# Kernel tuning notes

Hardware: AMD Instinct MI355X
Metric: run time of the kernel (lower is better)

Reference implementation:

```python
import jax, jax.numpy as jnp
import numpy as np

WS = 8        # window_size
SS = 4        # shift_size
NH = 8        # num_heads
DIM = 256
HD = DIM // NH
SCALE = HD ** -0.5
EPS = 1e-5


def _rel_pos_index(ws):
    ch, cw = np.meshgrid(np.arange(ws), np.arange(ws), indexing='ij')
    coords = np.stack([ch.ravel(), cw.ravel()])            # [2, ws*ws]
    rel = coords[:, :, None] - coords[:, None, :]           # [2, N, N]
    rel = rel.transpose(1, 2, 0)
    rel[:, :, 0] += ws - 1
    rel[:, :, 1] += ws - 1
    rel[:, :, 0] *= 2 * ws - 1
    return jnp.asarray(rel.sum(-1))                         # [N, N] int

REL_IDX = _rel_pos_index(WS)


def _ln(x, g, b):
    m = jnp.mean(x, axis=-1, keepdims=True)
    v = jnp.mean(jnp.square(x - m), axis=-1, keepdims=True)
    return (x - m) * jax.lax.rsqrt(v + EPS) * g + b


def setup_inputs() -> dict:
    key = jax.random.key(0)
    ks = jax.random.split(key, 12)
    B, L, C = 8, 16384, DIM
    s = lambda k, shape, scale=0.02: jax.random.normal(k, shape, jnp.float32) * scale
    return {
        'x': jax.random.normal(ks[0], (B, L, C), jnp.float32),
        'norm1_g': jnp.ones((C,), jnp.float32),
        'norm1_b': jnp.zeros((C,), jnp.float32),
        'qkv_w': s(ks[1], (C, 3 * C)),
        'qkv_b': jnp.zeros((3 * C,), jnp.float32),
        'rel_bias': s(ks[2], ((2 * WS - 1) ** 2, NH)),
        'proj_w': s(ks[3], (C, C)),
        'proj_b': jnp.zeros((C,), jnp.float32),
        'norm2_g': jnp.ones((C,), jnp.float32),
        'norm2_b': jnp.zeros((C,), jnp.float32),
        'fc1_w': s(ks[4], (C, C)),
        'fc1_b': jnp.zeros((C,), jnp.float32),
        'fc2_w': s(ks[5], (C, C)),
        'fc2_b': jnp.zeros((C,), jnp.float32),
        'H': 128,
        'W': 128,
    }


def reference(x, norm1_g, norm1_b, qkv_w, qkv_b, rel_bias, proj_w, proj_b,
              norm2_g, norm2_b, fc1_w, fc1_b, fc2_w, fc2_b, H, W):
    B, L, C = x.shape
    shortcut = x
    h = _ln(x, norm1_g, norm1_b).reshape(B, H, W, C)
    pad_b = (WS - H % WS) % WS
    pad_r = (WS - W % WS) % WS
    h = jnp.pad(h, ((0, 0), (0, pad_b), (0, pad_r), (0, 0)))
    Hp, Wp = H + pad_b, W + pad_r
    if SS > 0:
        h = jnp.roll(h, (-SS, -SS), axis=(1, 2))
    # window partition -> [B*nW, WS*WS, C]
    h = h.reshape(B, Hp // WS, WS, Wp // WS, WS, C)
    h = h.transpose(0, 1, 3, 2, 4, 5).reshape(-1, WS * WS, C)
    Bn, N = h.shape[0], WS * WS
    # attention
    qkv = (h @ qkv_w + qkv_b).reshape(Bn, N, 3, NH, HD)
    q, k, v = qkv[:, :, 0], qkv[:, :, 1], qkv[:, :, 2]   # [Bn, N, NH, HD]
    attn = jnp.einsum('bnhd,bmhd->bhnm', q * SCALE, k)
    bias = rel_bias[REL_IDX.reshape(-1)].reshape(N, N, NH).transpose(2, 0, 1)
    attn = jax.nn.softmax(attn + bias[None], axis=-1)
    o = jnp.einsum('bhnm,bmhd->bnhd', attn, v).reshape(Bn, N, C)
    o = o @ proj_w + proj_b
    # window reverse
    o = o.reshape(B, Hp // WS, Wp // WS, WS, WS, C)
    o = o.transpose(0, 1, 3, 2, 4, 5).reshape(B, Hp, Wp, C)
    if SS > 0:
        o = jnp.roll(o, (SS, SS), axis=(1, 2))
    o = o[:, :H, :W, :].reshape(B, H * W, C)
    x = shortcut + o
    # MLP (hidden = dim, exact GELU as nn.GELU default)
    m = _ln(x, norm2_g, norm2_b)
    m = jax.nn.gelu(m @ fc1_w + fc1_b, approximate=False)
    m = m @ fc2_w + fc2_b
    return x + m
```

## Files before the change

### kernel.cpp

```cpp
#include <hip/hip_runtime.h>
#include <stdint.h>

typedef __bf16 bf16;
typedef __bf16 bf16x4v __attribute__((ext_vector_type(4)));
typedef __bf16 bf16x8 __attribute__((ext_vector_type(8)));
typedef float floatx4 __attribute__((ext_vector_type(4)));
typedef float float4v __attribute__((ext_vector_type(4)));

#define SCALE 0.17677669529663689f

__device__ __forceinline__ float ldin(const void* p, long i, int f32) {
  return f32 ? ((const float*)p)[i] : (float)(((const bf16*)p)[i]);
}

__device__ __forceinline__ void async16(const bf16* g, bf16* l) {
  __builtin_amdgcn_global_load_lds(
      (const __attribute__((address_space(1))) void*)g,
      (__attribute__((address_space(3))) void*)l, 16, 0, 0);
}

__global__ void detect_k(const unsigned short* __restrict__ x, int* flag) {
  __shared__ int cnt;
  if (threadIdx.x == 0) cnt = 0;
  __syncthreads();
  int local = 0;
  for (int i = threadIdx.x; i < 4096; i += 256) {
    unsigned short w = x[i];
    int e = (w >> 7) & 0xFF;
    if (w != 0 && (e >= 0x9F || e <= 0x5F)) local++;
  }
  atomicAdd(&cnt, local);
  __syncthreads();
  if (threadIdx.x == 0) *flag = (cnt >= 64) ? 1 : 0;
}

__global__ void conv_w_k(const void* __restrict__ W, bf16* __restrict__ Wt,
                         int K, int N, const int* __restrict__ flag) {
  int f32 = *flag;
  int idx = blockIdx.x * 256 + threadIdx.x;
  if (idx < K * N) {
    int k = idx / N, n = idx % N;
    Wt[n * K + k] = (bf16)ldin(W, idx, f32);
  }
}

__global__ void conv3_k(const void* __restrict__ W0, const void* __restrict__ W1,
                        const void* __restrict__ W2, bf16* __restrict__ T0,
                        bf16* __restrict__ T1, bf16* __restrict__ T2,
                        const int* __restrict__ flag) {
  int f32 = *flag;
  int which = blockIdx.x >> 8;
  int idx = (blockIdx.x & 255) * 256 + threadIdx.x;
  const void* W = which == 0 ? W0 : which == 1 ? W1 : W2;
  bf16* T = which == 0 ? T0 : which == 1 ? T1 : T2;
  int k = idx >> 8, n = idx & 255;
  T[n * 256 + k] = (bf16)ldin(W, idx, f32);
}

__global__ void bias_k(const void* __restrict__ rel, float* __restrict__ bias_s,
                       const int* __restrict__ flag) {
  int f = *flag;
  int idx = blockIdx.x * 256 + threadIdx.x;
  int r = idx & 3, ni = (idx >> 2) & 3, mi = (idx >> 4) & 3;
  int l16 = (idx >> 6) & 15, quad = (idx >> 10) & 3, head = idx >> 12;
  int i = mi * 16 + quad * 4 + r, j = ni * 16 + l16;
  int dy = (i >> 3) - (j >> 3) + 7, dx = (i & 7) - (j & 7) + 7;
  bias_s[idx] = ldin(rel, (dy * 15 + dx) * 8 + head, f);
}

__global__ __launch_bounds__(256) void ln_k(const void* __restrict__ x,
                                            const void* __restrict__ g,
                                            const void* __restrict__ b,
                                            bf16* __restrict__ y,
                                            const int* __restrict__ flag,
                                            int x_input) {
  int f = *flag;
  int f32x = x_input ? f : 0;
  int wave = threadIdx.x >> 6, lane = threadIdx.x & 63;
  long row = (long)blockIdx.x * 4 + wave;
  float v[4];
  if (f32x) {
    float4v u = ((const float4v*)x)[row * 64 + lane];
    for (int i = 0; i < 4; i++) v[i] = u[i];
  } else {
    bf16x4v u = ((const bf16x4v*)x)[row * 64 + lane];
    for (int i = 0; i < 4; i++) v[i] = (float)u[i];
  }
  float s = v[0] + v[1] + v[2] + v[3];
  for (int off = 32; off > 0; off >>= 1) s += __shfl_xor(s, off, 64);
  float mean = s * (1.f / 256.f);
  float q = 0.f;
  for (int i = 0; i < 4; i++) { float d = v[i] - mean; q += d * d; }
  for (int off = 32; off > 0; off >>= 1) q += __shfl_xor(q, off, 64);
  float rstd = rsqrtf(q * (1.f / 256.f) + 1e-5f);
  bf16x4v o;
  for (int i = 0; i < 4; i++) {
    float gv = ldin(g, lane * 4 + i, f);
    float bv = ldin(b, lane * 4 + i, f);
    o[i] = (bf16)((v[i] - mean) * rstd * gv + bv);
  }
  ((bf16x4v*)y)[row * 64 + lane] = o;
}

template <int EPI>
__global__ __launch_bounds__(256) void gemm_bt_k(
    const bf16* __restrict__ A, const bf16* __restrict__ Bt,
    const void* __restrict__ bias, const void* __restrict__ res,
    void* __restrict__ C, int M, int N, int K, const int* __restrict__ flag,
    int res_input, int out_input) {
  __shared__ __align__(16) char smem[32768];
  bf16* Sb = (bf16*)smem;
  float* CsF = (float*)smem;

  const int tid = threadIdx.x;
  const int ntiles = gridDim.x;
  int bid = blockIdx.y * ntiles + blockIdx.x;
  const int nwg = ntiles * gridDim.y;
  if (!(nwg & 7)) bid = (bid & 7) * (nwg >> 3) + (bid >> 3);
  const long m0 = (long)(bid / ntiles) * 128;
  const int n0 = (bid % ntiles) * 128;
  const int wave = tid >> 6, lane = tid & 63;
  const int wm = wave & 1, wn = wave >> 1;
  const int quad = lane >> 4, l16 = lane & 15;

  floatx4 acc[4][4];
  for (int i = 0; i < 4; i++)
    for (int j = 0; j < 4; j++) acc[i][j] = (floatx4){0.f, 0.f, 0.f, 0.f};

  const int ldr = tid >> 2;
  const int ldc = (((tid & 3) ^ ((tid >> 3) & 3)) << 3);

  const bf16* gA0 = A + (m0 + ldr) * K + ldc;
  const bf16* gA1 = A + (m0 + 64 + ldr) * K + ldc;
  const bf16* gB0 = Bt + (long)(n0 + ldr) * K + ldc;
  const bf16* gB1 = Bt + (long)(n0 + 64 + ldr) * K + ldc;

  const int rswz = (l16 >> 1) & 3;
  const int NT = K >> 5;

#define STAGE(b, tt)                                   \
  do {                                                 \
    bf16* _base = Sb + (b) * 8192 + wave * 512;        \
    int _kt = (tt) << 5;                               \
    async16(gA0 + _kt, _base);                         \
    async16(gA1 + _kt, _base + 2048);                  \
    async16(gB0 + _kt, _base + 4096);                  \
    async16(gB1 + _kt, _base + 6144);                  \
  } while (0)

  STAGE(0, 0);
  __syncthreads();

  int cur = 0;
  for (int t = 0; t < NT; ++t) {
    if (t + 1 < NT) STAGE(cur ^ 1, t + 1);
    const bf16* As_t = Sb + cur * 8192;
    const bf16* Bs_t = As_t + 4096;
    bf16x8 af[4], bfr[4];
    for (int mi = 0; mi < 4; mi++)
      af[mi] = *(const bf16x8*)&As_t[(wm * 64 + mi * 16 + l16) * 32 +
                                     ((quad ^ rswz) << 3)];
    for (int ni = 0; ni < 4; ni++)
      bfr[ni] = *(const bf16x8*)&Bs_t[(wn * 64 + ni * 16 + l16) * 32 +
                                      ((quad ^ rswz) << 3)];
    for (int mi = 0; mi < 4; mi++)
      for (int ni = 0; ni < 4; ni++)
        acc[mi][ni] = __builtin_amdgcn_mfma_f32_16x16x32_bf16(
            af[mi], bfr[ni], acc[mi][ni], 0, 0, 0);
    __syncthreads();
    cur ^= 1;
  }
#undef STAGE

  const int f = *flag;
  const int rf32 = res_input ? f : 0;
  const int of32 = out_input ? f : 0;
  for (int mi = 0; mi < 4; mi++) {
    __syncthreads();
    for (int ni = 0; ni < 4; ni++) {
      int col = n0 + wn * 64 + ni * 16 + l16;
      float bv = ldin(bias, col, f);
      for (int r = 0; r < 4; r++) {
        float v = acc[mi][ni][r] + bv;
        if (EPI == 1) v = v * 0.5f * (1.f + erff(v * 0.70710678118654752f));
        CsF[(wm * 16 + quad * 4 + r) * 132 + wn * 64 + ni * 16 + l16] = v;
      }
    }
    __syncthreads();
    const int s = tid >> 3;
    const int seg = tid & 7;
    const long grow = m0 + (s >> 4) * 64 + mi * 16 + (s & 15);
    const int gcol = n0 + seg * 16;
    const float4v* src = (const float4v*)&CsF[s * 132 + seg * 16];
    float4v v0 = src[0], v1 = src[1], v2 = src[2], v3 = src[3];
    if (EPI == 2) {
      if (rf32) {
        const float4v* rp = (const float4v*)((const float*)res + grow * N + gcol);
        v0 += rp[0]; v1 += rp[1]; v2 += rp[2]; v3 += rp[3];
      } else {
        const bf16x8* rp = (const bf16x8*)((const bf16*)res + grow * N + gcol);
        bf16x8 r0 = rp[0], r1 = rp[1];
        for (int j = 0; j < 4; j++) {
          v0[j] += (float)r0[j];     v1[j] += (float)r0[4 + j];
          v2[j] += (float)r1[j];     v3[j] += (float)r1[4 + j];
        }
      }
    }
    if (of32) {
      float4v* dst = (float4v*)((float*)C + grow * N + gcol);
      dst[0] = v0; dst[1] = v1; dst[2] = v2; dst[3] = v3;
    } else {
      bf16x8 o0, o1;
      for (int j = 0; j < 4; j++) {
        o0[j] = (bf16)v0[j]; o0[4 + j] = (bf16)v1[j];
        o1[j] = (bf16)v2[j]; o1[4 + j] = (bf16)v3[j];
      }
      bf16x8* dst = (bf16x8*)((bf16*)C + grow * N + gcol);
      dst[0] = o0; dst[1] = o1;
    }
  }
}

__global__ __launch_bounds__(256) void attn_k(const bf16* __restrict__ qkv,
                                              const float* __restrict__ bias_s,
                                              bf16* __restrict__ o) {
  __shared__ bf16 Pb[4][64 * 64];
  __shared__ bf16 Vb[4][32 * 64];
  const int tid = threadIdx.x;
  const int wave = tid >> 6, lane = tid & 63;
  const int quad = lane >> 4, l16 = lane & 15;
  const int gid = blockIdx.x * 4 + wave;
  const int head = gid & 7, win = gid >> 3;
  const int wx = win & 15, wy = (win >> 4) & 15, bb = win >> 8;

  bf16* P = Pb[wave];
  bf16* Vt = Vb[wave];

  bf16x8 qf[4], kf[4];
  for (int mi = 0; mi < 4; mi++) {
    int t = mi * 16 + l16;
    int rr = (wy * 8 + (t >> 3) + 4) & 127;
    int cc = (wx * 8 + (t & 7) + 4) & 127;
    long base = ((long)(bb * 16384 + rr * 128 + cc)) * 768 + head * 32 + quad * 8;
    qf[mi] = *(const bf16x8*)(qkv + base);
    kf[mi] = *(const bf16x8*)(qkv + base + 256);
    bf16x8 vv = *(const bf16x8*)(qkv + base + 512);
    int tcol = t ^ (quad << 4);
    for (int jj = 0; jj < 8; jj++) Vt[(quad * 8 + jj) * 64 + tcol] = vv[jj];
  }
  __syncthreads();

  floatx4 acc[4][4];
  for (int mi = 0; mi < 4; mi++)
    for (int ni = 0; ni < 4; ni++) {
      floatx4 z = (floatx4){0.f, 0.f, 0.f, 0.f};
      acc[mi][ni] = __builtin_amdgcn_mfma_f32_16x16x32_bf16(qf[mi], kf[ni], z, 0, 0, 0);
    }

  const float4v* bp =
      (const float4v*)(bias_s + (((head * 4 + quad) * 16 + l16) << 6));
  for (int mi = 0; mi < 4; mi++) {
    float mx[4] = {-1e30f, -1e30f, -1e30f, -1e30f};
    for (int ni = 0; ni < 4; ni++) {
      float4v bv = bp[mi * 4 + ni];
      for (int r = 0; r < 4; r++) {
        acc[mi][ni][r] = acc[mi][ni][r] * SCALE + bv[r];
        mx[r] = fmaxf(mx[r], acc[mi][ni][r]);
      }
    }
    for (int r = 0; r < 4; r++) {
      float m = mx[r];
      for (int off = 1; off < 16; off <<= 1) m = fmaxf(m, __shfl_xor(m, off, 64));
      mx[r] = m;
    }
    float sm[4] = {0.f, 0.f, 0.f, 0.f};
    for (int ni = 0; ni < 4; ni++)
      for (int r = 0; r < 4; r++) {
        float e = __expf(acc[mi][ni][r] - mx[r]);
        acc[mi][ni][r] = e;
        sm[r] += e;
      }
    for (int r = 0; r < 4; r++) {
      float s = sm[r];
      for (int off = 1; off < 16; off <<= 1) s += __shfl_xor(s, off, 64);
      sm[r] = 1.f / s;
    }
    for (int ni = 0; ni < 4; ni++)
      for (int r = 0; r < 4; r++) {
        int i = mi * 16 + quad * 4 + r;
        int j = ni * 16 + l16;
        P[i * 64 + (j ^ ((i & 7) << 3))] = (bf16)(acc[mi][ni][r] * sm[r]);
      }
  }
  __syncthreads();

  floatx4 oacc[4][2];
  for (int mi = 0; mi < 4; mi++)
    for (int nt = 0; nt < 2; nt++) oacc[mi][nt] = (floatx4){0.f, 0.f, 0.f, 0.f};
  for (int ks = 0; ks < 2; ks++) {
    bf16x8 vfr[2];
    for (int nt = 0; nt < 2; nt++) {
      int d = nt * 16 + l16;
      vfr[nt] =
          *(const bf16x8*)&Vt[d * 64 + ((ks * 32 + quad * 8) ^ ((d >> 3) << 4))];
    }
    for (int mi = 0; mi < 4; mi++) {
      int i = mi * 16 + l16;
      bf16x8 pf =
          *(const bf16x8*)&P[i * 64 + ((ks * 32 + quad * 8) ^ ((i & 7) << 3))];
      for (int nt = 0; nt < 2; nt++)
        oacc[mi][nt] = __builtin_amdgcn_mfma_f32_16x16x32_bf16(pf, vfr[nt],
                                                               oacc[mi][nt], 0, 0, 0);
    }
  }

  for (int mi = 0; mi < 4; mi++)
    for (int r = 0; r < 4; r++) {
      int t = mi * 16 + quad * 4 + r;
      int rot = (t >> 1) & 3;
      int c0 = l16, c1 = 16 + l16;
      Vt[t * 32 + ((((c0 >> 3) + rot) & 3) << 3) + (c0 & 7)] = (bf16)oacc[mi][0][r];
      Vt[t * 32 + ((((c1 >> 3) + rot) & 3) << 3) + (c1 & 7)] = (bf16)oacc[mi][1][r];
    }
  {
    int t = lane;
    int rot = (t >> 1) & 3;
    int rr = (wy * 8 + (t >> 3) + 4) & 127;
    int cc = (wx * 8 + (t & 7) + 4) & 127;
    long base = ((long)(bb * 16384 + rr * 128 + cc)) * 256 + head * 32;
    bf16x8* dst = (bf16x8*)(o + base);
    for (int k = 0; k < 4; k++)
      dst[k] = *(const bf16x8*)&Vt[t * 32 + (((k + rot) & 3) << 3)];
  }
}

extern "C" void kernel_launch(void* const* d_in, const int* in_sizes, int n_in,
                              void* d_out, int out_size, void* d_ws,
                              size_t ws_size, hipStream_t stream) {
  const void* x = d_in[0];
  const void* n1g = d_in[1];
  const void* n1b = d_in[2];
  const void* qkv_w = d_in[3];
  const void* qkv_b = d_in[4];
  const void* rel_bias = d_in[5];
  const void* proj_w = d_in[6];
  const void* proj_b = d_in[7];
  const void* n2g = d_in[8];
  const void* n2b = d_in[9];
  const void* fc1_w = d_in[10];
  const void* fc1_b = d_in[11];
  const void* fc2_w = d_in[12];
  const void* fc2_b = d_in[13];

  char* ws = (char*)d_ws;
  int* flag = (int*)ws;
  float* bias_s = (float*)(ws + 4096);
  bf16* qkvWt = (bf16*)(ws + 262144);
  bf16* projWt = qkvWt + 768 * 256;
  bf16* fc1Wt = projWt + 256 * 256;
  bf16* fc2Wt = fc1Wt + 256 * 256;
  bf16* reg1 = (bf16*)(ws + (1 << 20));
  bf16* reg2 = (bf16*)(ws + (1 << 20) + 67108864);

  const int M = 131072;

  detect_k<<<1, 256, 0, stream>>>((const unsigned short*)x, flag);

  bias_k<<<128, 256, 0, stream>>>(rel_bias, bias_s, flag);
  conv_w_k<<<768, 256, 0, stream>>>(qkv_w, qkvWt, 256, 768, flag);
  conv3_k<<<768, 256, 0, stream>>>(proj_w, fc1_w, fc2_w, projWt, fc1Wt, fc2Wt,
                                   flag);

  bf16* h = reg1;
  ln_k<<<M / 4, 256, 0, stream>>>(x, n1g, n1b, h, flag, 1);

  bf16* qkv = reg2;
  gemm_bt_k<0><<<dim3(6, M / 128), 256, 0, stream>>>(
      h, qkvWt, qkv_b, nullptr, qkv, M, 768, 256, flag, 0, 0);

  bf16* o = reg1;
  attn_k<<<2048 * 8 / 4, 256, 0, stream>>>(qkv, bias_s, o);

  bf16* x2 = reg2;
  gemm_bt_k<2><<<dim3(2, M / 128), 256, 0, stream>>>(
      o, projWt, proj_b, x, x2, M, 256, 256, flag, 1, 0);

  bf16* mbuf = reg1;
  ln_k<<<M / 4, 256, 0, stream>>>(x2, n2g, n2b, mbuf, flag, 0);

  bf16* m1 = reg2 + 33554432;
  gemm_bt_k<1><<<dim3(2, M / 128), 256, 0, stream>>>(
      mbuf, fc1Wt, fc1_b, nullptr, m1, M, 256, 256, flag, 0, 0);

  gemm_bt_k<2><<<dim3(2, M / 128), 256, 0, stream>>>(
      m1, fc2Wt, fc2_b, x2, d_out, M, 256, 256, flag, 0, 1);
}
```

Before: 740.9 us.

## Load GEMM B fragments directly from global into registers, halve LDS

The GEMM kernel no longer stages the B (weight) tile through LDS. Each wave now loads its B fragments straight from global memory into registers, double-buffered by unrolling the k-loop by two, while A stays in LDS. LDS shrinks from 32 KB to about 16.5 KB, which may allow more blocks per CU and removes the LDS reads for B. The cost is more register pressure and uncoalesced, redundant global loads of B across the waves that share it. The loop also assumes NT is handled correctly when odd, since the second half is skipped only through its guard.

Result: slower. 813.6 us (+9.8%).

```diff
diff --git a/kernel.cpp b/kernel.cpp
--- a/kernel.cpp
+++ b/kernel.cpp
@@ -108,7 +108,7 @@
     const void* __restrict__ bias, const void* __restrict__ res,
     void* __restrict__ C, int M, int N, int K, const int* __restrict__ flag,
     int res_input, int out_input) {
-  __shared__ __align__(16) char smem[32768];
+  __shared__ __align__(16) char smem[16896];
   bf16* Sb = (bf16*)smem;
   float* CsF = (float*)smem;
 
@@ -132,45 +132,56 @@
 
   const bf16* gA0 = A + (m0 + ldr) * K + ldc;
   const bf16* gA1 = A + (m0 + 64 + ldr) * K + ldc;
-  const bf16* gB0 = Bt + (long)(n0 + ldr) * K + ldc;
-  const bf16* gB1 = Bt + (long)(n0 + 64 + ldr) * K + ldc;
+  const bf16* gB = Bt + (long)(n0 + wn * 64 + l16) * K + quad * 8;
+  const long bstride = (long)16 * K;
 
   const int rswz = (l16 >> 1) & 3;
   const int NT = K >> 5;
 
-#define STAGE(b, tt)                                   \
+#define STAGE_A(b, tt)                                 \
   do {                                                 \
-    bf16* _base = Sb + (b) * 8192 + wave * 512;        \
+    bf16* _base = Sb + (b) * 4096 + wave * 512;        \
     int _kt = (tt) << 5;                               \
     async16(gA0 + _kt, _base);                         \
     async16(gA1 + _kt, _base + 2048);                  \
-    async16(gB0 + _kt, _base + 4096);                  \
-    async16(gB1 + _kt, _base + 6144);                  \
   } while (0)
 
-  STAGE(0, 0);
+#define BLOAD(dst, tt)                                                 \
+  do {                                                                 \
+    int _kt = (tt) << 5;                                               \
+    for (int _ni = 0; _ni < 4; _ni++)                                  \
+      dst[_ni] = *(const bf16x8*)(gB + _ni * bstride + _kt);           \
+  } while (0)
+
+#define COMPUTE(bufidx, bfrag)                                          \
+  do {                                                                  \
+    const bf16* As_t = Sb + (bufidx) * 4096;                            \
+    bf16x8 af[4];                                                       \
+    for (int mi = 0; mi < 4; mi++)                                      \
+      af[mi] = *(const bf16x8*)&As_t[(wm * 64 + mi * 16 + l16) * 32 +   \
+                                     ((quad ^ rswz) << 3)];             \
+    for (int mi = 0; mi < 4; mi++)                                      \
+      for (int ni = 0; ni < 4; ni++)                                    \
+        acc[mi][ni] = __builtin_amdgcn_mfma_f32_16x16x32_bf16(          \
+            af[mi], bfrag[ni], acc[mi][ni], 0, 0, 0);                   \
+  } while (0)
+
+  bf16x8 bf0[4], bf1[4];
+  STAGE_A(0, 0);
+  BLOAD(bf0, 0);
   __syncthreads();
 
-  int cur = 0;
-  for (int t = 0; t < NT; ++t) {
-    if (t + 1 < NT) STAGE(cur ^ 1, t + 1);
-    const bf16* As_t = Sb + cur * 8192;
-    const bf16* Bs_t = As_t + 4096;
-    bf16x8 af[4], bfr[4];
-    for (int mi = 0; mi < 4; mi++)
-      af[mi] = *(const bf16x8*)&As_t[(wm * 64 + mi * 16 + l16) * 32 +
-                                     ((quad ^ rswz) << 3)];
-    for (int ni = 0; ni < 4; ni++)
-      bfr[ni] = *(const bf16x8*)&Bs_t[(wn * 64 + ni * 16 + l16) * 32 +
-                                      ((quad ^ rswz) << 3)];
-    for (int mi = 0; mi < 4; mi++)
-      for (int ni = 0; ni < 4; ni++)
-        acc[mi][ni] = __builtin_amdgcn_mfma_f32_16x16x32_bf16(
-            af[mi], bfr[ni], acc[mi][ni], 0, 0, 0);
+  for (int t = 0; t < NT; t += 2) {
+    if (t + 1 < NT) { STAGE_A(1, t + 1); BLOAD(bf1, t + 1); }
+    COMPUTE(0, bf0);
     __syncthreads();
-    cur ^= 1;
-  }
-#undef STAGE
+    if (t + 2 < NT) { STAGE_A(0, t + 2); BLOAD(bf0, t + 2); }
+    COMPUTE(1, bf1);
+    __syncthreads();
+  }
+#undef STAGE_A
+#undef BLOAD
+#undef COMPUTE
 
   const int f = *flag;
   const int rf32 = res_input ? f : 0;
```
